# Optimization experiments

Hardware: AMD Instinct MI355X
Metric: run time of the kernel (lower is better)

Reference implementation:

```python
import jax, jax.numpy as jnp
import numpy as np

TOP_K = 2

def setup_inputs() -> dict:
    key = jax.random.key(0)
    k1, k2 = jax.random.split(key)
    D, E = 4096, 64
    hidden_states = jax.random.normal(k1, (2, 8192, D), dtype=jnp.float32)
    W = jax.random.normal(k2, (E, D), dtype=jnp.float32) / np.sqrt(D)
    b = jnp.zeros((E,), dtype=jnp.float32)
    return {"hidden_states": hidden_states, "W": W, "b": b}

def reference(hidden_states, W, b):
    # gate: logits [B, S, E]
    logits = jnp.einsum('bsd,ed->bse', hidden_states, W) + b
    scores = jax.nn.softmax(logits, axis=-1)
    top_k_values, top_k_indices = jax.lax.top_k(scores, TOP_K)
    return ((top_k_indices, top_k_values), scores)
```

## Files before the change

### kernel.cpp

```cpp
#include <hip/hip_runtime.h>
#include <math.h>

#define D_DIM 4096
#define E_DIM 64
#define TM 64
#define BK 64
#define NC (D_DIM / BK)
#define TP 68
#define LP 65

__global__ __launch_bounds__(256, 1) void router_kernel(
    const float* __restrict__ hs,
    const float* __restrict__ W,
    const float* __restrict__ bias,
    float* __restrict__ out,
    int nTok)
{
    __shared__ float hsT[BK * TP];
    __shared__ float wT [BK * TP];
    __shared__ float lg [TM * LP];
    __shared__ float s_m[TM];
    __shared__ float s_inv[TM];

    const int tid   = threadIdx.x;
    const int tBase = blockIdx.x * TM;

    const int ty = tid >> 4;
    const int tx = tid & 15;

    const int ld_d = tid & 63;
    const int ld_g = tid >> 6;

    float4 ph[4], pw[4];
    float acc[4][4];
    #pragma unroll
    for (int i = 0; i < 4; ++i)
        #pragma unroll
        for (int j = 0; j < 4; ++j)
            acc[i][j] = 0.f;

    const float* hsB = hs + (size_t)tBase * D_DIM;

    auto g_load = [&](int c) {
        const int d = c * BK + ld_d;
        #pragma unroll
        for (int p = 0; p < 4; ++p) {
            const int t0 = ld_g * 16 + p * 4;
            ph[p].x = hsB[(size_t)(t0 + 0) * D_DIM + d];
            ph[p].y = hsB[(size_t)(t0 + 1) * D_DIM + d];
            ph[p].z = hsB[(size_t)(t0 + 2) * D_DIM + d];
            ph[p].w = hsB[(size_t)(t0 + 3) * D_DIM + d];
            pw[p].x = W[(size_t)(t0 + 0) * D_DIM + d];
            pw[p].y = W[(size_t)(t0 + 1) * D_DIM + d];
            pw[p].z = W[(size_t)(t0 + 2) * D_DIM + d];
            pw[p].w = W[(size_t)(t0 + 3) * D_DIM + d];
        }
    };

    auto l_store = [&]() {
        #pragma unroll
        for (int p = 0; p < 4; ++p) {
            const int t0 = ld_g * 16 + p * 4;
            *(float4*)&hsT[ld_d * TP + t0] = ph[p];
            *(float4*)&wT [ld_d * TP + t0] = pw[p];
        }
    };

    auto compute = [&]() {
        #pragma unroll
        for (int kk = 0; kk < BK; ++kk) {
            const float4 a = *(const float4*)&hsT[kk * TP + ty * 4];
            const float4 w = *(const float4*)&wT [kk * TP + tx * 4];
            const float av[4] = {a.x, a.y, a.z, a.w};
            const float wv[4] = {w.x, w.y, w.z, w.w};
            #pragma unroll
            for (int i = 0; i < 4; ++i)
                #pragma unroll
                for (int j = 0; j < 4; ++j)
                    acc[i][j] = fmaf(av[i], wv[j], acc[i][j]);
        }
    };

    g_load(0);
    l_store();
    __syncthreads();
    for (int c = 0; c < NC - 1; ++c) {
        g_load(c + 1);
        compute();
        __syncthreads();
        l_store();
        __syncthreads();
    }
    compute();

    #pragma unroll
    for (int i = 0; i < 4; ++i)
        #pragma unroll
        for (int j = 0; j < 4; ++j)
            lg[(ty * 4 + i) * LP + (tx * 4 + j)] = acc[i][j] + bias[tx * 4 + j];
    __syncthreads();

    float* out_idx = out;
    float* out_val = out + (size_t)nTok * 2;
    float* out_sc  = out + (size_t)nTok * 4;

    if (tid < TM) {
        const int t = tid;
        const float* row = &lg[t * LP];
        float m = row[0];
        #pragma unroll
        for (int e = 1; e < E_DIM; ++e) m = fmaxf(m, row[e]);
        float sum = 0.f;
        float b1 = -INFINITY, b2 = -INFINITY;
        int i1 = 0, i2 = 0;
        for (int e = 0; e < E_DIM; ++e) {
            const float l = row[e];
            sum += __expf(l - m);
            if (l > b1)      { b2 = b1; i2 = i1; b1 = l; i1 = e; }
            else if (l > b2) { b2 = l; i2 = e; }
        }
        const float inv = 1.f / sum;
        s_m[t]   = m;
        s_inv[t] = inv;
        const size_t gt = (size_t)(tBase + t);
        out_idx[gt * 2 + 0] = (float)i1;
        out_idx[gt * 2 + 1] = (float)i2;
        out_val[gt * 2 + 0] = __expf(b1 - m) * inv;
        out_val[gt * 2 + 1] = __expf(b2 - m) * inv;
    }
    __syncthreads();

    const int e  = tid & 63;
    const int tq = tid >> 6;
    #pragma unroll
    for (int p = 0; p < 16; ++p) {
        const int t = p * 4 + tq;
        out_sc[(size_t)(tBase + t) * E_DIM + e] =
            __expf(lg[t * LP + e] - s_m[t]) * s_inv[t];
    }
}

extern "C" void kernel_launch(void* const* d_in, const int* in_sizes, int n_in,
                              void* d_out, int out_size, void* d_ws, size_t ws_size,
                              hipStream_t stream) {
    const float* hs = (const float*)d_in[0];
    const float* W  = (const float*)d_in[1];
    const float* b  = (const float*)d_in[2];
    float* out = (float*)d_out;
    const int nTok = in_sizes[0] / D_DIM;
    dim3 grid(nTok / TM), block(256);
    router_kernel<<<grid, block, 0, stream>>>(hs, W, b, out, nTok);
}
```

Baseline: 460.1 us.

## Split-K the router GEMM with atomics and a separate softmax/top-k epilogue kernel

Splits the 4096-long reduction into four parts so four times as many blocks run, raises the occupancy hint, and switches global loads to coalesced float4 reads along D. Partial logits are accumulated with float atomics into the scores output buffer after a memset, and a second kernel adds bias and does softmax, top-2 and score writes. This adds a memset, an extra launch and atomic traffic, and makes summation order nondeterministic.

Measured after the change: 446.1 us. -3.0%, faster.

```diff
diff --git a/kernel.cpp b/kernel.cpp
--- a/kernel.cpp
+++ b/kernel.cpp
@@ -5,31 +5,31 @@
 #define E_DIM 64
 #define TM 64
 #define BK 64
-#define NC (D_DIM / BK)
+#define KSPLIT 4
+#define KPART (D_DIM / KSPLIT)
+#define KCH (KPART / BK)
 #define TP 68
 #define LP 65
 
-__global__ __launch_bounds__(256, 1) void router_kernel(
+__global__ __launch_bounds__(256, 4) void router_gemm(
     const float* __restrict__ hs,
     const float* __restrict__ W,
-    const float* __restrict__ bias,
-    float* __restrict__ out,
+    float* __restrict__ logits,
     int nTok)
 {
     __shared__ float hsT[BK * TP];
     __shared__ float wT [BK * TP];
-    __shared__ float lg [TM * LP];
-    __shared__ float s_m[TM];
-    __shared__ float s_inv[TM];
 
     const int tid   = threadIdx.x;
-    const int tBase = blockIdx.x * TM;
+    const int part  = blockIdx.x & (KSPLIT - 1);
+    const int tBase = (blockIdx.x >> 2) * TM;
+    const int kBase = part * KPART;
 
     const int ty = tid >> 4;
     const int tx = tid & 15;
 
-    const int ld_d = tid & 63;
-    const int ld_g = tid >> 6;
+    const int dq = tid & 15;
+    const int r  = tid >> 4;
 
     float4 ph[4], pw[4];
     float acc[4][4];
@@ -39,30 +39,28 @@
         for (int j = 0; j < 4; ++j)
             acc[i][j] = 0.f;
 
-    const float* hsB = hs + (size_t)tBase * D_DIM;
+    const float* hsB = hs + (size_t)tBase * D_DIM + kBase;
+    const float* WB  = W + kBase;
 
     auto g_load = [&](int c) {
-        const int d = c * BK + ld_d;
+        const int d = c * BK + dq * 4;
         #pragma unroll
         for (int p = 0; p < 4; ++p) {
-            const int t0 = ld_g * 16 + p * 4;
-            ph[p].x = hsB[(size_t)(t0 + 0) * D_DIM + d];
-            ph[p].y = hsB[(size_t)(t0 + 1) * D_DIM + d];
-            ph[p].z = hsB[(size_t)(t0 + 2) * D_DIM + d];
-            ph[p].w = hsB[(size_t)(t0 + 3) * D_DIM + d];
-            pw[p].x = W[(size_t)(t0 + 0) * D_DIM + d];
-            pw[p].y = W[(size_t)(t0 + 1) * D_DIM + d];
-            pw[p].z = W[(size_t)(t0 + 2) * D_DIM + d];
-            pw[p].w = W[(size_t)(t0 + 3) * D_DIM + d];
+            const int row = p * 16 + r;
+            ph[p] = *(const float4*)&hsB[(size_t)row * D_DIM + d];
+            pw[p] = *(const float4*)&WB [(size_t)row * D_DIM + d];
         }
     };
 
     auto l_store = [&]() {
         #pragma unroll
         for (int p = 0; p < 4; ++p) {
-            const int t0 = ld_g * 16 + p * 4;
-            *(float4*)&hsT[ld_d * TP + t0] = ph[p];
-            *(float4*)&wT [ld_d * TP + t0] = pw[p];
+            const int row = p * 16 + r;
+            #pragma unroll
+            for (int i = 0; i < 4; ++i) {
+                hsT[(dq * 4 + i) * TP + row] = ((const float*)&ph[p])[i];
+                wT [(dq * 4 + i) * TP + row] = ((const float*)&pw[p])[i];
+            }
         }
     };
 
@@ -84,7 +82,8 @@
     g_load(0);
     l_store();
     __syncthreads();
-    for (int c = 0; c < NC - 1; ++c) {
+    #pragma unroll 1
+    for (int c = 0; c < KCH - 1; ++c) {
         g_load(c + 1);
         compute();
         __syncthreads();
@@ -94,17 +93,44 @@
     compute();
 
     #pragma unroll
-    for (int i = 0; i < 4; ++i)
+    for (int i = 0; i < 4; ++i) {
+        const size_t rowOff = (size_t)(tBase + ty * 4 + i) * E_DIM + tx * 4;
         #pragma unroll
         for (int j = 0; j < 4; ++j)
-            lg[(ty * 4 + i) * LP + (tx * 4 + j)] = acc[i][j] + bias[tx * 4 + j];
-    __syncthreads();
+            unsafeAtomicAdd(&logits[rowOff + j], acc[i][j]);
+    }
+}
+
+__global__ __launch_bounds__(256, 4) void router_epilogue(
+    const float* __restrict__ bias,
+    float* __restrict__ out,
+    int nTok)
+{
+    __shared__ float lg[64 * LP];
+    __shared__ float s_m[64];
+    __shared__ float s_inv[64];
+
+    const int tid   = threadIdx.x;
+    const int tBase = blockIdx.x * 64;
 
     float* out_idx = out;
     float* out_val = out + (size_t)nTok * 2;
-    float* out_sc  = out + (size_t)nTok * 4;
+    float* sc      = out + (size_t)nTok * 4;
 
-    if (tid < TM) {
+    #pragma unroll
+    for (int p = 0; p < 4; ++p) {
+        const int f = p * 1024 + tid * 4;
+        const float4 v  = *(const float4*)&sc[(size_t)tBase * E_DIM + f];
+        const int t = f >> 6, e = f & 63;
+        const float4 bb = *(const float4*)&bias[e];
+        lg[t * LP + e + 0] = v.x + bb.x;
+        lg[t * LP + e + 1] = v.y + bb.y;
+        lg[t * LP + e + 2] = v.z + bb.z;
+        lg[t * LP + e + 3] = v.w + bb.w;
+    }
+    __syncthreads();
+
+    if (tid < 64) {
         const int t = tid;
         const float* row = &lg[t * LP];
         float m = row[0];
@@ -135,7 +161,7 @@
     #pragma unroll
     for (int p = 0; p < 16; ++p) {
         const int t = p * 4 + tq;
-        out_sc[(size_t)(tBase + t) * E_DIM + e] =
+        sc[(size_t)(tBase + t) * E_DIM + e] =
             __expf(lg[t * LP + e] - s_m[t]) * s_inv[t];
     }
 }
@@ -148,6 +174,13 @@
     const float* b  = (const float*)d_in[2];
     float* out = (float*)d_out;
     const int nTok = in_sizes[0] / D_DIM;
-    dim3 grid(nTok / TM), block(256);
-    router_kernel<<<grid, block, 0, stream>>>(hs, W, b, out, nTok);
+
+    float* logits = out + (size_t)nTok * 4;
+    hipMemsetAsync(logits, 0, (size_t)nTok * E_DIM * sizeof(float), stream);
+
+    dim3 g1(nTok / TM * KSPLIT), b1(256);
+    router_gemm<<<g1, b1, 0, stream>>>(hs, W, logits, nTok);
+
+    dim3 g2(nTok / 64), b2(256);
+    router_epilogue<<<g2, b2, 0, stream>>>(b, out, nTok);
 }
```
